# Optimization experiments

Measured on AMD Instinct MI355X. Metric: run time of the kernel, lower is better.

## Reference

```python
import jax, jax.numpy as jnp
from jax import lax
import numpy as np

T = 140
H = 64
B = 8192

def _uniform(key, shape, k):
    return jax.random.uniform(key, shape, dtype=jnp.float32, minval=-k, maxval=k)

def setup_inputs() -> dict:
    key = jax.random.key(0)
    ks = jax.random.split(key, 12)
    k = 1.0 / np.sqrt(H)  # torch default init bound
    return {
        "x": jax.random.normal(ks[0], (B, T, 1), dtype=jnp.float32),
        "h_state": jnp.zeros((2, B, H), dtype=jnp.float32),
        "W_ih0": _uniform(ks[1], (H, 1), k),
        "W_hh0": _uniform(ks[2], (H, H), k),
        "b_ih0": _uniform(ks[3], (H,), k),
        "b_hh0": _uniform(ks[4], (H,), k),
        "W_ih1": _uniform(ks[5], (H, H), k),
        "W_hh1": _uniform(ks[6], (H, H), k),
        "b_ih1": _uniform(ks[7], (H,), k),
        "b_hh1": _uniform(ks[8], (H,), k),
        "W_out": _uniform(ks[9], (1, H), k),
        "b_out": _uniform(ks[10], (1,), k),
    }

def reference(x, h_state, W_ih0, W_hh0, b_ih0, b_hh0, W_ih1, W_hh1, b_ih1, b_hh1, W_out, b_out):
    b = x.shape[0]
    x = x.reshape(b, T, 1)
    xs = jnp.swapaxes(x, 0, 1)  # [T, B, 1]

    def step(carry, xt):
        h0, h1 = carry
        # torch RNN cell: h_t = tanh(x W_ih^T + b_ih + h_{t-1} W_hh^T + b_hh)
        h0n = jnp.tanh(xt @ W_ih0.T + b_ih0 + h0 @ W_hh0.T + b_hh0)
        h1n = jnp.tanh(h0n @ W_ih1.T + b_ih1 + h1 @ W_hh1.T + b_hh1)
        return (h0n, h1n), h1n

    (hf0, hf1), ys = lax.scan(step, (h_state[0], h_state[1]), xs)
    ys = jnp.swapaxes(ys, 0, 1)  # [B, T, H]
    out = (ys @ W_out.T + b_out).reshape(b, T, 1)
    h_final = jnp.stack([hf0, hf1])  # [2, B, H]
    return out, h_final
```

## Files before the change

kernel.cpp:

```cpp
#include <hip/hip_runtime.h>

#define TT 140
#define BB 8192
#define HH 64
#define BT 16
#define K_TANH 2.88539008178f

typedef _Float16 half4 __attribute__((ext_vector_type(4)));
typedef float    f32x4 __attribute__((ext_vector_type(4)));

#define MFMA16(a,b,c) __builtin_amdgcn_mfma_f32_16x16x16f16(a, b, c, 0, 0, 0)

__device__ __forceinline__ float tanh_ps(float as) {
    float e = __builtin_amdgcn_exp2f(as);
    return 1.0f - 2.0f * __builtin_amdgcn_rcpf(e + 1.0f);
}

__device__ __forceinline__ half4 ldw4(const float* p, float s) {
    f32x4 w = *(const f32x4*)p;
    half4 h;
    #pragma unroll
    for (int i = 0; i < 4; ++i) h[i] = (_Float16)(s * w[i]);
    return h;
}

__global__ __launch_bounds__(128, 1)
void rnn_kernel(const float* __restrict__ x,
                const float* __restrict__ h_state,
                const float* __restrict__ W_ih0,
                const float* __restrict__ W_hh0,
                const float* __restrict__ b_ih0,
                const float* __restrict__ b_hh0,
                const float* __restrict__ W_ih1,
                const float* __restrict__ W_hh1,
                const float* __restrict__ b_ih1,
                const float* __restrict__ b_hh1,
                const float* __restrict__ W_out,
                const float* __restrict__ b_out,
                float* __restrict__ out)
{
    __shared__ float xs[TT * 17];
    __shared__ f32x4 ei[2][4][64];

    const int tid  = threadIdx.x;
    const int wid  = tid >> 6;
    const int lane = tid & 63;
    const int n    = lane & 15;
    const int q    = lane >> 4;
    const int b0   = blockIdx.x * BT;

    half4 A0[4][4], AI[4][4], AH[4][4];
    float e00[4][4], e10[4][4], e01[4][4], WO[4][4];
    half4 H0[4], H1[4];
    float bout = 0.f;
    if (wid == 0) {
        #pragma unroll
        for (int g = 0; g < 4; ++g)
        #pragma unroll
        for (int kk = 0; kk < 4; ++kk) {
            const int off = (16 * g + n) * HH + 16 * kk + 4 * q;
            A0[g][kk] = ldw4(W_hh0 + off, K_TANH);
            AI[g][kk] = ldw4(W_ih1 + off, K_TANH);
        }
        #pragma unroll
        for (int g = 0; g < 4; ++g)
        #pragma unroll
        for (int r = 0; r < 4; ++r) {
            int j = 16 * g + 4 * q + r;
            e00[g][r] = K_TANH * (b_ih0[j] + b_hh0[j]);
            e10[g][r] = K_TANH * W_ih0[j];
        }
        #pragma unroll
        for (int kk = 0; kk < 4; ++kk)
            H0[kk] = ldw4(h_state + (size_t)(b0 + n) * HH + 16 * kk + 4 * q, 1.0f);
    } else {
        #pragma unroll
        for (int g = 0; g < 4; ++g)
        #pragma unroll
        for (int kk = 0; kk < 4; ++kk) {
            const int off = (16 * g + n) * HH + 16 * kk + 4 * q;
            AH[g][kk] = ldw4(W_hh1 + off, K_TANH);
        }
        #pragma unroll
        for (int g = 0; g < 4; ++g)
        #pragma unroll
        for (int r = 0; r < 4; ++r) {
            int j = 16 * g + 4 * q + r;
            e01[g][r] = K_TANH * (b_ih1[j] + b_hh1[j]);
            WO[g][r]  = W_out[j];
        }
        #pragma unroll
        for (int kk = 0; kk < 4; ++kk)
            H1[kk] = ldw4(h_state + (size_t)BB * HH + (size_t)(b0 + n) * HH
                                   + 16 * kk + 4 * q, 1.0f);
        bout = b_out[0];
    }

    for (int i = tid; i < TT * BT; i += 128) {
        int t = i >> 4, b = i & 15;
        xs[t * 17 + b] = x[(size_t)(b0 + b) * TT + t];
    }
    __syncthreads();

    for (int p = 0; p <= TT; ++p) {
        if (wid == 0) {
            if (p < TT) {
                float xt = xs[p * 17 + n];
                f32x4 d[4];
                #pragma unroll
                for (int g = 0; g < 4; ++g) {
                    f32x4 c;
                    #pragma unroll
                    for (int r = 0; r < 4; ++r) c[r] = e00[g][r] + e10[g][r] * xt;
                    #pragma unroll
                    for (int kk = 0; kk < 4; ++kk) c = MFMA16(A0[g][kk], H0[kk], c);
                    d[g] = c;
                }
                #pragma unroll
                for (int g = 0; g < 4; ++g) {
                    half4 h;
                    #pragma unroll
                    for (int r = 0; r < 4; ++r) h[r] = (_Float16)tanh_ps(d[g][r]);
                    H0[g] = h;
                }
                #pragma unroll
                for (int g = 0; g < 4; ++g) {
                    f32x4 c = {0.f, 0.f, 0.f, 0.f};
                    #pragma unroll
                    for (int kk = 0; kk < 4; ++kk) c = MFMA16(AI[g][kk], H0[kk], c);
                    ei[p & 1][g][lane] = c;
                }
            }
        } else {
            if (p >= 1) {
                const int s = p - 1;
                f32x4 d[4];
                #pragma unroll
                for (int g = 0; g < 4; ++g) {
                    f32x4 ep = ei[s & 1][g][lane];
                    f32x4 c;
                    #pragma unroll
                    for (int r = 0; r < 4; ++r) c[r] = e01[g][r] + ep[r];
                    #pragma unroll
                    for (int kk = 0; kk < 4; ++kk) c = MFMA16(AH[g][kk], H1[kk], c);
                    d[g] = c;
                }
                float pr = 0.f;
                #pragma unroll
                for (int g = 0; g < 4; ++g) {
                    half4 h;
                    #pragma unroll
                    for (int r = 0; r < 4; ++r) {
                        float hn = tanh_ps(d[g][r]);
                        pr += hn * WO[g][r];
                        h[r] = (_Float16)hn;
                    }
                    H1[g] = h;
                }
                pr += __shfl_xor(pr, 16, 64);
                pr += __shfl_xor(pr, 32, 64);
                if (lane < 16) out[(size_t)(b0 + n) * TT + s] = pr + bout;
            }
        }
        __syncthreads();
    }

    const size_t OFF = (size_t)BB * TT;
    if (wid == 0) {
        #pragma unroll
        for (int kk = 0; kk < 4; ++kk) {
            f32x4 v;
            #pragma unroll
            for (int i = 0; i < 4; ++i) v[i] = (float)H0[kk][i];
            *(f32x4*)(out + OFF + (size_t)(b0 + n) * HH + 16 * kk + 4 * q) = v;
        }
    } else {
        #pragma unroll
        for (int kk = 0; kk < 4; ++kk) {
            f32x4 v;
            #pragma unroll
            for (int i = 0; i < 4; ++i) v[i] = (float)H1[kk][i];
            *(f32x4*)(out + OFF + (size_t)BB * HH + (size_t)(b0 + n) * HH
                               + 16 * kk + 4 * q) = v;
        }
    }
}

extern "C" void kernel_launch(void* const* d_in, const int* in_sizes, int n_in,
                              void* d_out, int out_size, void* d_ws, size_t ws_size,
                              hipStream_t stream) {
    const float* x      = (const float*)d_in[0];
    const float* hst    = (const float*)d_in[1];
    const float* W_ih0  = (const float*)d_in[2];
    const float* W_hh0  = (const float*)d_in[3];
    const float* b_ih0  = (const float*)d_in[4];
    const float* b_hh0  = (const float*)d_in[5];
    const float* W_ih1  = (const float*)d_in[6];
    const float* W_hh1  = (const float*)d_in[7];
    const float* b_ih1  = (const float*)d_in[8];
    const float* b_hh1  = (const float*)d_in[9];
    const float* W_out  = (const float*)d_in[10];
    const float* b_outp = (const float*)d_in[11];
    float* out = (float*)d_out;

    dim3 grid(BB / BT);
    dim3 block(128);
    rnn_kernel<<<grid, block, 0, stream>>>(x, hst, W_ih0, W_hh0, b_ih0, b_hh0,
                                           W_ih1, W_hh1, b_ih1, b_hh1,
                                           W_out, b_outp, out);
}
```

Baseline: 166.4 us.

## Batch RNN layer pipeline into 4-step windows and stage outputs in LDS

The two-wave layer pipeline now hands off work in windows of four timesteps, with a deeper LDS ring for the layer-1 input projections. This cuts block-wide barriers from one per timestep to one per window. Per-step output predictions are also buffered in shared memory and written to global memory in one coalesced pass at the end, replacing strided scalar stores. In exchange it uses more LDS and adds a longer pipeline fill and drain of one full window.

```diff
diff --git a/kernel.cpp b/kernel.cpp
--- a/kernel.cpp
+++ b/kernel.cpp
@@ -4,6 +4,7 @@
 #define BB 8192
 #define HH 64
 #define BT 16
+#define WIN 4
 #define K_TANH 2.88539008178f
 
 typedef _Float16 half4 __attribute__((ext_vector_type(4)));
@@ -40,7 +41,8 @@
                 float* __restrict__ out)
 {
     __shared__ float xs[TT * 17];
-    __shared__ f32x4 ei[2][4][64];
+    __shared__ float pps[TT * 17];
+    __shared__ f32x4 ei[2 * WIN][4][64];
 
     const int tid  = threadIdx.x;
     const int wid  = tid >> 6;
@@ -102,69 +104,82 @@
     }
     __syncthreads();
 
-    for (int p = 0; p <= TT; ++p) {
+    for (int win = 0; win <= TT / WIN; ++win) {
         if (wid == 0) {
-            if (p < TT) {
-                float xt = xs[p * 17 + n];
-                f32x4 d[4];
+            if (win < TT / WIN) {
                 #pragma unroll
-                for (int g = 0; g < 4; ++g) {
-                    f32x4 c;
-                    #pragma unroll
-                    for (int r = 0; r < 4; ++r) c[r] = e00[g][r] + e10[g][r] * xt;
-                    #pragma unroll
-                    for (int kk = 0; kk < 4; ++kk) c = MFMA16(A0[g][kk], H0[kk], c);
-                    d[g] = c;
-                }
-                #pragma unroll
-                for (int g = 0; g < 4; ++g) {
-                    half4 h;
-                    #pragma unroll
-                    for (int r = 0; r < 4; ++r) h[r] = (_Float16)tanh_ps(d[g][r]);
-                    H0[g] = h;
-                }
-                #pragma unroll
-                for (int g = 0; g < 4; ++g) {
-                    f32x4 c = {0.f, 0.f, 0.f, 0.f};
-                    #pragma unroll
-                    for (int kk = 0; kk < 4; ++kk) c = MFMA16(AI[g][kk], H0[kk], c);
-                    ei[p & 1][g][lane] = c;
+                for (int j = 0; j < WIN; ++j) {
+                    const int p  = WIN * win + j;
+                    const int pb = ((win & 1) ? WIN : 0) + j;
+                    float xt = xs[p * 17 + n];
+                    f32x4 d[4];
+                    #pragma unroll
+                    for (int g = 0; g < 4; ++g) {
+                        f32x4 c;
+                        #pragma unroll
+                        for (int r = 0; r < 4; ++r) c[r] = e00[g][r] + e10[g][r] * xt;
+                        #pragma unroll
+                        for (int kk = 0; kk < 4; ++kk) c = MFMA16(A0[g][kk], H0[kk], c);
+                        d[g] = c;
+                    }
+                    #pragma unroll
+                    for (int g = 0; g < 4; ++g) {
+                        half4 h;
+                        #pragma unroll
+                        for (int r = 0; r < 4; ++r) h[r] = (_Float16)tanh_ps(d[g][r]);
+                        H0[g] = h;
+                    }
+                    #pragma unroll
+                    for (int g = 0; g < 4; ++g) {
+                        f32x4 c = {0.f, 0.f, 0.f, 0.f};
+                        #pragma unroll
+                        for (int kk = 0; kk < 4; ++kk) c = MFMA16(AI[g][kk], H0[kk], c);
+                        ei[pb][g][lane] = c;
+                    }
                 }
             }
         } else {
-            if (p >= 1) {
-                const int s = p - 1;
-                f32x4 d[4];
+            if (win >= 1) {
                 #pragma unroll
-                for (int g = 0; g < 4; ++g) {
-                    f32x4 ep = ei[s & 1][g][lane];
-                    f32x4 c;
-                    #pragma unroll
-                    for (int r = 0; r < 4; ++r) c[r] = e01[g][r] + ep[r];
-                    #pragma unroll
-                    for (int kk = 0; kk < 4; ++kk) c = MFMA16(AH[g][kk], H1[kk], c);
-                    d[g] = c;
+                for (int j = 0; j < WIN; ++j) {
+                    const int s  = WIN * (win - 1) + j;
+                    const int sb = (((win - 1) & 1) ? WIN : 0) + j;
+                    f32x4 d[4];
+                    #pragma unroll
+                    for (int g = 0; g < 4; ++g) {
+                        f32x4 ep = ei[sb][g][lane];
+                        f32x4 c;
+                        #pragma unroll
+                        for (int r = 0; r < 4; ++r) c[r] = e01[g][r] + ep[r];
+                        #pragma unroll
+                        for (int kk = 0; kk < 4; ++kk) c = MFMA16(AH[g][kk], H1[kk], c);
+                        d[g] = c;
+                    }
+                    float pr = 0.f;
+                    #pragma unroll
+                    for (int g = 0; g < 4; ++g) {
+                        half4 h;
+                        #pragma unroll
+                        for (int r = 0; r < 4; ++r) {
+                            float hn = tanh_ps(d[g][r]);
+                            pr += hn * WO[g][r];
+                            h[r] = (_Float16)hn;
+                        }
+                        H1[g] = h;
+                    }
+                    pr += __shfl_xor(pr, 16, 64);
+                    pr += __shfl_xor(pr, 32, 64);
+                    if (lane < 16) pps[s * 17 + n] = pr + bout;
                 }
-                float pr = 0.f;
-                #pragma unroll
-                for (int g = 0; g < 4; ++g) {
-                    half4 h;
-                    #pragma unroll
-                    for (int r = 0; r < 4; ++r) {
-                        float hn = tanh_ps(d[g][r]);
-                        pr += hn * WO[g][r];
-                        h[r] = (_Float16)hn;
-                    }
-                    H1[g] = h;
-                }
-                pr += __shfl_xor(pr, 16, 64);
-                pr += __shfl_xor(pr, 32, 64);
-                if (lane < 16) out[(size_t)(b0 + n) * TT + s] = pr + bout;
             }
         }
         __syncthreads();
     }
 
+    for (int i = tid; i < TT * BT; i += 128) {
+        int t = i >> 4, b = i & 15;
+        out[(size_t)(b0 + b) * TT + t] = pps[t * 17 + b];
+    }
     const size_t OFF = (size_t)BB * TT;
     if (wid == 0) {
         #pragma unroll
```

Measured after the change: 170.8 us. +2.7%, slower.
